# Kernel optimization log

Hardware: AMD Instinct MI355X
Metric: run time of the kernel (lower is better)

## Reference

```python
import jax, jax.numpy as jnp
from jax import lax
import numpy as np

B, T, H, L = 4096, 7, 512, 256
D = 2 * H  # bidirectional LSTM feature dim


def _lstm(x, wih, whh, bih, bhh, reverse):
    # x: [B, T, L]; torch gate order i, f, g, o
    b, hdim = x.shape[0], whh.shape[0]
    xs = jnp.swapaxes(x, 0, 1)  # [T, B, L]
    bias = bih + bhh

    def step(carry, xt):
        h, c = carry
        gates = xt @ wih + h @ whh + bias
        i, f, g, o = jnp.split(gates, 4, axis=-1)
        c = jax.nn.sigmoid(f) * c + jax.nn.sigmoid(i) * jnp.tanh(g)
        h = jax.nn.sigmoid(o) * jnp.tanh(c)
        return (h, c), h

    h0 = jnp.zeros((b, hdim), x.dtype)
    _, hs = lax.scan(step, (h0, h0), xs, reverse=reverse)
    return jnp.swapaxes(hs, 0, 1)  # [B, T, H]


def _att(enc, dec):
    # Sequential attention: keys/values start as enc and grow with each decoder output.
    keys = enc  # [B, T, D]
    outs = []
    for i in range(dec.shape[1]):  # fixed small T=7, Python loop is static
        q = dec[:, i, :]                                  # [B, D]
        scores = jnp.einsum('bd,btd->bt', q, keys)        # dot over features
        a = jax.nn.softmax(scores, axis=1)
        ctx = jnp.einsum('bt,btd->bd', a, keys)
        out = ctx + q
        outs.append(out)
        keys = jnp.concatenate([keys, out[:, None, :]], axis=1)
    return jnp.stack(outs, axis=1)  # [B, T, D]


def _deconv(x, w, b):
    # torch ConvTranspose2d (stride 1, pad 0) == full conv with flipped, in/out-swapped kernel
    kh, kw = w.shape[2], w.shape[3]
    w2 = jnp.transpose(w[:, :, ::-1, ::-1], (1, 0, 2, 3))  # [out, in, kh, kw]
    y = lax.conv_general_dilated(x, w2, (1, 1), ((kh - 1, kh - 1), (kw - 1, kw - 1)),
                                 dimension_numbers=('NCHW', 'OIHW', 'NCHW'))
    return y + b[None, :, None, None]


def setup_inputs() -> dict:
    key = jax.random.key(0)
    ks = jax.random.split(key, 12)
    p = lambda k, shape: jax.random.normal(k, shape, jnp.float32) * 0.02
    return {
        'lstm_enc': jax.random.normal(ks[0], (B, T, D), jnp.float32),
        'gaussian_noise': jax.random.normal(ks[1], (B, L), jnp.float32),
        'embedrep_w': p(ks[2], (L, L * T)), 'embedrep_b': jnp.zeros((L * T,), jnp.float32),
        'wih_f': p(ks[3], (L, 4 * H)), 'whh_f': p(ks[4], (H, 4 * H)),
        'bih_f': jnp.zeros((4 * H,), jnp.float32), 'bhh_f': jnp.zeros((4 * H,), jnp.float32),
        'wih_b': p(ks[5], (L, 4 * H)), 'whh_b': p(ks[6], (H, 4 * H)),
        'bih_b': jnp.zeros((4 * H,), jnp.float32), 'bhh_b': jnp.zeros((4 * H,), jnp.float32),
        'emb_w': p(ks[7], (D, 1024)), 'emb_b': jnp.zeros((1024,), jnp.float32),
        'dc3_w': p(ks[8], (64, 32, 1, 3)), 'dc3_b': jnp.zeros((32,), jnp.float32),
        'dc1_w': p(ks[9], (32, 16, 1, 5)), 'dc1_b': jnp.zeros((16,), jnp.float32),
        'dc2_w': p(ks[10], (16, 1, 3, 3)), 'dc2_b': jnp.zeros((1,), jnp.float32),
        'infer': 0,
    }


def reference(lstm_enc, gaussian_noise, embedrep_w, embedrep_b,
              wih_f, whh_f, bih_f, bhh_f, wih_b, whh_b, bih_b, bhh_b,
              emb_w, emb_b, dc3_w, dc3_b, dc1_w, dc1_b, dc2_w, dc2_b, infer):
    b = lstm_enc.shape[0]
    g1 = jax.nn.soft_sign(gaussian_noise @ embedrep_w + embedrep_b)   # [B, L*T]
    rep = g1.reshape(b, T, L)                                          # [B, 7, L]
    hf = _lstm(rep, wih_f, whh_f, bih_f, bhh_f, False)
    hb = _lstm(rep, wih_b, whh_b, bih_b, bhh_b, True)
    lstm1 = jnp.concatenate([hf, hb], axis=-1)                         # [B, 7, 2H]
    att_out = _att(lstm_enc, lstm1)                                    # [B, 7, 2H]
    emb = att_out @ emb_w + emb_b                                      # [B, 7, 1024]
    up = jax.nn.soft_sign(emb).reshape(b * T, 64, 1, 16)
    x = jax.nn.leaky_relu(_deconv(up, dc3_w, dc3_b))                   # [B*7, 32, 1, 18]
    x = jax.nn.leaky_relu(_deconv(x, dc1_w, dc1_b))                    # [B*7, 16, 1, 22]
    x = jax.nn.leaky_relu(_deconv(x, dc2_w, dc2_b))                    # [B*7, 1, 3, 24]
    x = jax.nn.softmax(x, axis=2)                                      # softmax over H dim (=3)
    out = x.reshape(b, T, 1, 3, 24)[:, :, -1, :, :]                    # [B, 7, 3, 24]
    return out
```

## Files before the change

kernel.cpp:

```cpp
#include <hip/hip_runtime.h>
#include <stdint.h>


typedef __attribute__((ext_vector_type(4))) float f32x4;
typedef __attribute__((ext_vector_type(8))) short bf16x8;
typedef __attribute__((ext_vector_type(4))) unsigned short us4;

__device__ __forceinline__ unsigned short f2b(float f) {
  union { float f; unsigned u; } x; x.f = f;
  unsigned r = x.u + 0x7FFFu + ((x.u >> 16) & 1u);
  return (unsigned short)(r >> 16);
}
__device__ __forceinline__ float b2f(unsigned short s) {
  union { unsigned u; float f; } x; x.u = ((unsigned)s) << 16; return x.f;
}
__device__ __forceinline__ float sigmoidf(float x) {
  return 1.f / (1.f + __expf(-x));
}
__device__ __forceinline__ float fast_tanh(float x) {
  x = fminf(15.f, fmaxf(-15.f, x));
  float e = __expf(2.f * x);
  return (e - 1.f) / (e + 1.f);
}

__device__ __forceinline__ void gl_lds16(const void* g, void* l) {
  auto gp = reinterpret_cast<const __attribute__((address_space(1))) unsigned int*>(
      reinterpret_cast<uintptr_t>(g));
  auto lp = reinterpret_cast<__attribute__((address_space(3))) unsigned int*>(
      reinterpret_cast<uintptr_t>(l));
  __builtin_amdgcn_global_load_lds(gp, lp, 16, 0, 0);
}


__device__ __forceinline__ void stage_half(const unsigned short* src, int ld,
                                           unsigned short* hbase, int tid) {
  const int row_in = tid >> 2;
  const int gidx = tid & 3;
#pragma unroll
  for (int r = 0; r < 2; ++r) {
    int row = r * 128 + row_in;
    int gsrc = gidx ^ ((row >> 1) & 3);
    gl_lds16(src + (size_t)row * ld + gsrc * 8, hbase + r * 4096 + (tid >> 6) * 512);
  }
}

__device__ __forceinline__ bf16x8 lds_fragH(const unsigned short* hbase, int row, int lq) {
  return *(const bf16x8*)(hbase + row * 32 + (lq ^ (((row >> 1) & 3) << 3)));
}

__device__ __forceinline__ void tile_reads(const unsigned short* Ab, const unsigned short* Bb,
                                           int wm, int wn, int lane,
                                           bf16x8 (&a)[8], bf16x8 (&b)[4]) {
  const int lr = lane & 15, lq = (lane >> 4) * 8;
#pragma unroll
  for (int i = 0; i < 8; ++i) a[i] = lds_fragH(Ab, wm * 128 + i * 16 + lr, lq);
#pragma unroll
  for (int n = 0; n < 4; ++n) b[n] = lds_fragH(Bb, wn * 64 + n * 16 + lr, lq);
}

__device__ __forceinline__ void tile_mfma(bf16x8 (&a)[8], bf16x8 (&b)[4], f32x4 (&acc)[8][4]) {
  __builtin_amdgcn_s_setprio(1);
#pragma unroll
  for (int i = 0; i < 8; ++i)
#pragma unroll
    for (int n = 0; n < 4; ++n)
      acc[i][n] = __builtin_amdgcn_mfma_f32_16x16x32_bf16(a[i], b[n], acc[i][n], 0, 0, 0);
  __builtin_amdgcn_s_setprio(0);
}

#define RING_TOP(t, NT)                                                   \
  if ((t) < (NT)-2) asm volatile("s_waitcnt vmcnt(4)" ::: "memory");      \
  else              asm volatile("s_waitcnt vmcnt(0)" ::: "memory");      \
  __builtin_amdgcn_s_barrier();                                           \
  __builtin_amdgcn_sched_barrier(0);                                      \
  asm volatile("s_waitcnt lgkmcnt(0)" ::: "memory");                      \
  __builtin_amdgcn_sched_barrier(0);

__device__ __forceinline__ void stage128x64(const unsigned short* src, int ld,
                                            unsigned short* lds, int wv, int lane) {
#pragma unroll
  for (int r = 0; r < 4; ++r) {
    int row = r * 32 + wv * 8 + (lane >> 3);
    gl_lds16(src + (size_t)row * ld + (lane & 7) * 8, lds + (r * 32 + wv * 8) * 64);
  }
}
__device__ __forceinline__ void mfma_tile(const unsigned short* As, const unsigned short* Bs,
                                          int wm, int wn, int lane, f32x4 acc[4][4]) {
#pragma unroll
  for (int kk = 0; kk < 2; ++kk) {
    int ko = kk * 32 + (lane >> 4) * 8;
    bf16x8 a[4], b[4];
#pragma unroll
    for (int i = 0; i < 4; ++i)
      a[i] = *(const bf16x8*)(As + (size_t)(wm * 64 + i * 16 + (lane & 15)) * 64 + ko);
#pragma unroll
    for (int i = 0; i < 4; ++i)
      b[i] = *(const bf16x8*)(Bs + (size_t)(wn * 64 + i * 16 + (lane & 15)) * 64 + ko);
#pragma unroll
    for (int mi = 0; mi < 4; ++mi)
#pragma unroll
      for (int ni = 0; ni < 4; ++ni)
        acc[mi][ni] = __builtin_amdgcn_mfma_f32_16x16x32_bf16(a[mi], b[ni], acc[mi][ni], 0, 0, 0);
  }
}

__global__ __launch_bounds__(256) void pack_kernel(
    const float* __restrict__ noise, const float* __restrict__ erep_w,
    const float* __restrict__ emb_w,
    const float* __restrict__ wih_f, const float* __restrict__ whh_f,
    const float* __restrict__ bih_f, const float* __restrict__ bhh_f,
    const float* __restrict__ wih_b, const float* __restrict__ whh_b,
    const float* __restrict__ bih_b, const float* __restrict__ bhh_b,
    unsigned short* __restrict__ noiseb, unsigned short* __restrict__ erepT,
    unsigned short* __restrict__ embT, unsigned short* __restrict__ lstmW,
    float* __restrict__ lstmB) {
  const int N0 = 4096 * 256;
  const int N1 = 1792 * 256;
  const int N2 = 1024 * 1024;
  const int N3 = 2 * 2048 * 768;
  const int N4 = 2 * 2048;
  const int total = N0 + N1 + N2 + N3 + N4;
  for (int i = blockIdx.x * 256 + threadIdx.x; i < total; i += gridDim.x * 256) {
    int x = i;
    if (x < N0) { noiseb[x] = f2b(noise[x]); continue; }
    x -= N0;
    if (x < N1) { int n = x >> 8, k = x & 255; erepT[x] = f2b(erep_w[k * 1792 + n]); continue; }
    x -= N1;
    if (x < N2) {
      int n = x >> 10, k = x & 1023;
      int o = (n & 63) * 16 + (n >> 6);
      embT[x] = f2b(emb_w[k * 1024 + o]);
      continue;
    }
    x -= N2;
    if (x < N3) {
      int dir = x / (2048 * 768);
      int r = x - dir * (2048 * 768);
      int npk = r / 768, k = r - (r / 768) * 768;
      int blk = npk >> 6, g = (npk >> 4) & 3, u = npk & 15;
      int o = g * 512 + blk * 16 + u;
      const float* wih = dir ? wih_b : wih_f;
      const float* whh = dir ? whh_b : whh_f;
      float v = (k < 256) ? wih[k * 2048 + o] : whh[(k - 256) * 2048 + o];
      lstmW[x] = f2b(v);
      continue;
    }
    x -= N3;
    {
      int dir = x >> 11, npk = x & 2047;
      int blk = npk >> 6, g = (npk >> 4) & 3, u = npk & 15;
      int o = g * 512 + blk * 16 + u;
      lstmB[x] = dir ? (bih_b[o] + bhh_b[o]) : (bih_f[o] + bhh_f[o]);
    }
  }
}

__global__ __launch_bounds__(256) void gemm_rep_kernel(
    const unsigned short* __restrict__ A, const unsigned short* __restrict__ Bt,
    const float* __restrict__ bias, unsigned short* __restrict__ rep_t) {
  __shared__ unsigned short As[128 * 64];
  __shared__ unsigned short Bs[128 * 64];
  const int lane = threadIdx.x & 63, wv = threadIdx.x >> 6;
  const int wm = wv >> 1, wn = wv & 1;
  const int m0 = blockIdx.y * 128, n0 = blockIdx.x * 128;
  f32x4 acc[4][4];
#pragma unroll
  for (int i = 0; i < 4; ++i)
#pragma unroll
    for (int j = 0; j < 4; ++j) acc[i][j] = (f32x4){0.f, 0.f, 0.f, 0.f};
  for (int k0 = 0; k0 < 256; k0 += 64) {
    stage128x64(A + (size_t)m0 * 256 + k0, 256, As, wv, lane);
    stage128x64(Bt + (size_t)n0 * 256 + k0, 256, Bs, wv, lane);
    __syncthreads();
    mfma_tile(As, Bs, wm, wn, lane, acc);
    __syncthreads();
  }
#pragma unroll
  for (int ni = 0; ni < 4; ++ni) {
    int n = n0 + wn * 64 + ni * 16 + (lane & 15);
    float bv = bias[n];
    int t = n >> 8, l = n & 255;
#pragma unroll
    for (int mi = 0; mi < 4; ++mi)
#pragma unroll
      for (int r = 0; r < 4; ++r) {
        int m = m0 + wm * 64 + mi * 16 + (lane >> 4) * 4 + r;
        float v = acc[mi][ni][r] + bv;
        v = v / (1.f + fabsf(v));
        rep_t[((size_t)t * 4096 + m) * 256 + l] = f2b(v);
      }
  }
}

__global__ __launch_bounds__(512, 2) void lstm_step256_kernel(
    const unsigned short* __restrict__ rep_t, const unsigned short* __restrict__ Wp,
    const float* __restrict__ biasP, unsigned short* __restrict__ hbuf,
    unsigned short* __restrict__ cbuf, unsigned short* __restrict__ lstm1, int step) {
  __shared__ unsigned short Ar[4][8192];
  __shared__ unsigned short Br[4][8192];
  const int tid = threadIdx.x, lane = tid & 63, wv = tid >> 6;
  const int wm = wv >> 2, wn = wv & 3;
  const int swz = (blockIdx.x & 7) * 32 + (blockIdx.x >> 3);
  const int dir = swz >> 7;
  const int by = (swz & 127) >> 3, bx = swz & 7;
  const int m0 = by * 256, n0 = bx * 256;
  const int t_proc = dir ? (6 - step) : step;
  const unsigned short* W = Wp + (size_t)dir * 2048 * 768;
  const unsigned short* hin = hbuf + ((size_t)(step & 1) * 2 + dir) * (4096 * 512);
  unsigned short* hout = hbuf + ((size_t)((step + 1) & 1) * 2 + dir) * (4096 * 512);
  unsigned short* cp = cbuf + (size_t)dir * (4096 * 512);
  const unsigned short* xsrc = rep_t + (size_t)t_proc * 4096 * 256;

  f32x4 acc[8][4];
#pragma unroll
  for (int i = 0; i < 8; ++i)
#pragma unroll
    for (int j = 0; j < 4; ++j) acc[i][j] = (f32x4){0.f, 0.f, 0.f, 0.f};

  auto asrc = [&](int tt) {
    return tt < 8 ? xsrc + (size_t)m0 * 256 + tt * 32
                  : hin + (size_t)m0 * 512 + (tt - 8) * 32;
  };
  auto ald = [&](int tt) { return tt < 8 ? 256 : 512; };

  stage_half(asrc(0), ald(0), Ar[0], tid);
  stage_half(W + (size_t)n0 * 768 + 0 * 32, 768, Br[0], tid);
  stage_half(asrc(1), ald(1), Ar[1], tid);
  stage_half(W + (size_t)n0 * 768 + 1 * 32, 768, Br[1], tid);
  stage_half(asrc(2), ald(2), Ar[2], tid);
  stage_half(W + (size_t)n0 * 768 + 2 * 32, 768, Br[2], tid);
  asm volatile("s_waitcnt vmcnt(8)" ::: "memory");
  __builtin_amdgcn_s_barrier();
  __builtin_amdgcn_sched_barrier(0);
  bf16x8 a[8], b[4];
  tile_reads(Ar[0], Br[0], wm, wn, lane, a, b);

  for (int t = 0; t < 24; ++t) {
    RING_TOP(t, 24)
    tile_mfma(a, b, acc);
    if (t + 3 < 24) {
      stage_half(asrc(t + 3), ald(t + 3), Ar[(t + 3) & 3], tid);
      stage_half(W + (size_t)n0 * 768 + (t + 3) * 32, 768, Br[(t + 3) & 3], tid);
    }
    if (t + 1 < 24) tile_reads(Ar[(t + 1) & 3], Br[(t + 1) & 3], wm, wn, lane, a, b);
  }

  const int u = lane & 15;
  const int blk = (n0 + wn * 64) >> 6;
  const int j = blk * 16 + u;
  const float bz0 = biasP[dir * 2048 + blk * 64 + 0 * 16 + u];
  const float bz1 = biasP[dir * 2048 + blk * 64 + 1 * 16 + u];
  const float bz2 = biasP[dir * 2048 + blk * 64 + 2 * 16 + u];
  const float bz3 = biasP[dir * 2048 + blk * 64 + 3 * 16 + u];
#pragma unroll
  for (int mi = 0; mi < 8; ++mi)
#pragma unroll
    for (int r = 0; r < 4; ++r) {
      int row = m0 + wm * 128 + mi * 16 + (lane >> 4) * 4 + r;
      float gi = acc[mi][0][r] + bz0;
      float gf = acc[mi][1][r] + bz1;
      float gg = acc[mi][2][r] + bz2;
      float go = acc[mi][3][r] + bz3;
      size_t ci = (size_t)row * 512 + j;
      float c = sigmoidf(gf) * b2f(cp[ci]) + sigmoidf(gi) * fast_tanh(gg);
      cp[ci] = f2b(c);
      float h = sigmoidf(go) * fast_tanh(c);
      unsigned short hb = f2b(h);
      hout[ci] = hb;
      lstm1[((size_t)row * 7 + t_proc) * 1024 + dir * 512 + j] = hb;
    }
}

__global__ __launch_bounds__(256) void att_fused3_kernel(
    const float* __restrict__ enc, const unsigned short* __restrict__ lstm1,
    unsigned short* __restrict__ att) {
  __shared__ unsigned short Qs[7 * 1032];
  __shared__ unsigned short Es[7 * 1032];
  __shared__ float P[8 * 256];
  __shared__ float sG[98];
  __shared__ float sC[7][14];
  __shared__ float sA[16];
  const int tid = threadIdx.x, lane = tid & 63, wv = tid >> 6;
  const int b = blockIdx.x;
  const float* Eb = enc + (size_t)b * 7168;
  const unsigned short* Qb = lstm1 + (size_t)b * 7168;

  if (tid < 98) ((float*)sC)[tid] = 0.f;

  const f32x4* Eb4 = (const f32x4*)Eb;
  const int d0 = tid * 4;
#pragma unroll
  for (int r = 0; r < 7; ++r) {
    f32x4 v = Eb4[r * 256 + tid];
    us4 hi;
#pragma unroll
    for (int e = 0; e < 4; ++e) hi[e] = f2b(v[e]);
    *(us4*)&Es[r * 1032 + d0] = hi;
    *(us4*)&Qs[r * 1032 + d0] = *(const us4*)(Qb + r * 1024 + d0);
  }
  asm volatile("s_waitcnt lgkmcnt(0)" ::: "memory");
  __builtin_amdgcn_sched_barrier(0);

  {
    const int rr = lane & 15;
    const int rowc = rr % 7;
    const int kbase = wv * 256 + (lane >> 4) * 8;
    f32x4 g1 = {0.f, 0.f, 0.f, 0.f}, g2 = {0.f, 0.f, 0.f, 0.f};
#pragma unroll
    for (int s = 0; s < 8; ++s) {
      const int k0 = kbase + s * 32;
      bf16x8 aq = *(const bf16x8*)&Qs[rowc * 1032 + k0];
      bf16x8 be = *(const bf16x8*)&Es[rowc * 1032 + k0];
      g1 = __builtin_amdgcn_mfma_f32_16x16x32_bf16(aq, be, g1, 0, 0, 0);
      g2 = __builtin_amdgcn_mfma_f32_16x16x32_bf16(aq, aq, g2, 0, 0, 0);
    }
    *(f32x4*)&P[((wv * 2 + 0) * 64 + lane) * 4] = g1;
    *(f32x4*)&P[((wv * 2 + 1) * 64 + lane) * 4] = g2;
  }
  __syncthreads();

  if (tid < 98) {
    int i = tid / 14, v = tid - i * 14;
    int col = v < 7 ? v : v - 7;
    int tile = v < 7 ? 0 : 1;
    int ln = ((i >> 2) << 4) | col;
    int rg = i & 3;
    float s = 0.f;
#pragma unroll
    for (int w = 0; w < 4; ++w) s += P[((w * 2 + tile) * 64 + ln) * 4 + rg];
    sG[i * 14 + v] = s;
  }
  __syncthreads();
  if (wv == 0) {
    for (int i = 0; i < 7; ++i) {
      const int nt = 7 + i;
      float s = -1e30f;
      if (lane < 7) {
        s = sG[i * 14 + lane];
      } else if (lane < nt) {
        int jj = lane - 7;
        float a2 = 0.f;
#pragma unroll
        for (int v = 0; v < 14; ++v) a2 += sC[jj][v] * sG[i * 14 + v];
        s = a2;
      }
      float mx = s;
#pragma unroll
      for (int off = 8; off >= 1; off >>= 1) mx = fmaxf(mx, __shfl_xor(mx, off, 16));
      float e = (lane < nt) ? __expf(s - mx) : 0.f;
      float sum = e;
#pragma unroll
      for (int off = 8; off >= 1; off >>= 1) sum += __shfl_xor(sum, off, 16);
      float aw = e / sum;
      if (lane < 16) sA[lane] = aw;
      if (lane < 14) {
        float c = (lane < 7) ? sA[lane] : 0.f;
        for (int jj = 0; jj < i; ++jj) c += sA[7 + jj] * sC[jj][lane];
        if (lane == 7 + i) c += 1.f;
        sC[i][lane] = c;
      }
    }
  }
  __syncthreads();

  {
    float acc[7][4];
#pragma unroll
    for (int i = 0; i < 7; ++i)
#pragma unroll
      for (int e = 0; e < 4; ++e) acc[i][e] = 0.f;
#pragma unroll
    for (int t = 0; t < 7; ++t) {
      us4 ev = *(const us4*)&Es[t * 1032 + d0];
      float evf[4];
#pragma unroll
      for (int e = 0; e < 4; ++e) evf[e] = b2f(ev[e]);
#pragma unroll
      for (int i = 0; i < 7; ++i) {
        float c = sC[i][t];
#pragma unroll
        for (int e = 0; e < 4; ++e) acc[i][e] += c * evf[e];
      }
    }
#pragma unroll
    for (int m = 0; m < 7; ++m) {
      us4 qv = *(const us4*)&Qs[m * 1032 + d0];
      float qf[4];
#pragma unroll
      for (int e = 0; e < 4; ++e) qf[e] = b2f(qv[e]);
#pragma unroll
      for (int i = m; i < 7; ++i) {
        float c = sC[i][7 + m];
#pragma unroll
        for (int e = 0; e < 4; ++e) acc[i][e] += c * qf[e];
      }
    }
    unsigned short* Ab = att + (size_t)b * 7168;
#pragma unroll
    for (int i = 0; i < 7; ++i) {
      us4 r;
#pragma unroll
      for (int e = 0; e < 4; ++e) r[e] = f2b(acc[i][e]);
      *(us4*)(Ab + i * 1024 + d0) = r;
    }
  }
}

__global__ __launch_bounds__(512, 2) void gemm_emb256_kernel(
    const unsigned short* __restrict__ A, const unsigned short* __restrict__ Bt,
    const float* __restrict__ bias, unsigned short* __restrict__ up_t) {
  __shared__ unsigned short Ar[4][8192];
  __shared__ unsigned short Br[4][8192];
  const int tid = threadIdx.x, lane = tid & 63, wv = tid >> 6;
  const int wm = wv >> 2, wn = wv & 3;
  const int swz = (blockIdx.x & 7) * 56 + (blockIdx.x >> 3);
  const int by = swz >> 2, bx = swz & 3;
  const int m0 = by * 256, n0 = bx * 256;

  f32x4 acc[8][4];
#pragma unroll
  for (int i = 0; i < 8; ++i)
#pragma unroll
    for (int j = 0; j < 4; ++j) acc[i][j] = (f32x4){0.f, 0.f, 0.f, 0.f};

  const unsigned short* Abase = A + (size_t)m0 * 1024;
  const unsigned short* Bbase = Bt + (size_t)n0 * 1024;

  stage_half(Abase + 0 * 32, 1024, Ar[0], tid);
  stage_half(Bbase + 0 * 32, 1024, Br[0], tid);
  stage_half(Abase + 1 * 32, 1024, Ar[1], tid);
  stage_half(Bbase + 1 * 32, 1024, Br[1], tid);
  stage_half(Abase + 2 * 32, 1024, Ar[2], tid);
  stage_half(Bbase + 2 * 32, 1024, Br[2], tid);
  asm volatile("s_waitcnt vmcnt(8)" ::: "memory");
  __builtin_amdgcn_s_barrier();
  __builtin_amdgcn_sched_barrier(0);
  bf16x8 a[8], b[4];
  tile_reads(Ar[0], Br[0], wm, wn, lane, a, b);

  for (int t = 0; t < 32; ++t) {
    RING_TOP(t, 32)
    tile_mfma(a, b, acc);
    if (t + 3 < 32) {
      stage_half(Abase + (t + 3) * 32, 1024, Ar[(t + 3) & 3], tid);
      stage_half(Bbase + (t + 3) * 32, 1024, Br[(t + 3) & 3], tid);
    }
    if (t + 1 < 32) tile_reads(Ar[(t + 1) & 3], Br[(t + 1) & 3], wm, wn, lane, a, b);
  }

#pragma unroll
  for (int ni = 0; ni < 4; ++ni) {
    int np = n0 + wn * 64 + ni * 16 + (lane & 15);
    int o = (np & 63) * 16 + (np >> 6);
    float bv = bias[o];
#pragma unroll
    for (int mi = 0; mi < 8; ++mi)
#pragma unroll
      for (int r = 0; r < 4; ++r) {
        int m = m0 + wm * 128 + mi * 16 + (lane >> 4) * 4 + r;
        float v = acc[mi][ni][r] + bv;
        v = v / (1.f + fabsf(v));
        up_t[(size_t)m * 1024 + np] = f2b(v);
      }
  }
}

__global__ __launch_bounds__(256) void dc3_kernel(const unsigned short* __restrict__ up_t,
                                                  const float* __restrict__ w3,
                                                  const float* __restrict__ b3,
                                                  unsigned short* __restrict__ y1_t) {
  const int lane = threadIdx.x & 63, wv = threadIdx.x >> 6;
  const int kq = (lane >> 4) * 8;
  const int oc = lane & 15;
  bf16x8 bf[2][6];
#pragma unroll
  for (int nt = 0; nt < 2; ++nt)
#pragma unroll
    for (int kk = 0; kk < 6; ++kk) {
      bf16x8 v;
#pragma unroll
      for (int t = 0; t < 8; ++t) {
        int k = kk * 32 + kq + t;
        int jj = k >> 6, ic = k & 63;
        v[t] = (short)f2b(w3[((size_t)ic * 32 + nt * 16 + oc) * 3 + jj]);
      }
      bf[nt][kk] = v;
    }
  const float bia0 = b3[oc], bia1 = b3[16 + oc];
  const int base_chunk = blockIdx.x * 32 + wv * 8;
  for (int cc = 0; cc < 8; ++cc) {
    const int chunk = base_chunk + cc;
    int m = chunk * 16 + (lane & 15);
    int img = m / 18, ow = m - img * 18;
    const unsigned short* arow = up_t + (size_t)img * 1024;
    f32x4 acc0 = {0.f, 0.f, 0.f, 0.f}, acc1 = {0.f, 0.f, 0.f, 0.f};
#pragma unroll
    for (int kk = 0; kk < 6; ++kk) {
      int jj = kk >> 1;
      int ic0 = (kk & 1) * 32 + kq;
      int iw = ow - jj;
      bf16x8 a = {0, 0, 0, 0, 0, 0, 0, 0};
      if ((unsigned)iw < 16u) a = *(const bf16x8*)(arow + iw * 64 + ic0);
      acc0 = __builtin_amdgcn_mfma_f32_16x16x32_bf16(a, bf[0][kk], acc0, 0, 0, 0);
      acc1 = __builtin_amdgcn_mfma_f32_16x16x32_bf16(a, bf[1][kk], acc1, 0, 0, 0);
    }
#pragma unroll
    for (int r = 0; r < 4; ++r) {
      int mm = chunk * 16 + (lane >> 4) * 4 + r;
      float v0 = acc0[r] + bia0; v0 = v0 > 0.f ? v0 : 0.01f * v0;
      float v1 = acc1[r] + bia1; v1 = v1 > 0.f ? v1 : 0.01f * v1;
      y1_t[(size_t)mm * 32 + oc] = f2b(v0);
      y1_t[(size_t)mm * 32 + 16 + oc] = f2b(v1);
    }
  }
}

__global__ __launch_bounds__(256) void dc1_kernel(const unsigned short* __restrict__ y1_t,
                                                  const float* __restrict__ w1,
                                                  const float* __restrict__ b1,
                                                  unsigned short* __restrict__ y2_t) {
  const int lane = threadIdx.x & 63, wv = threadIdx.x >> 6;
  const int kq = (lane >> 4) * 8;
  const int oc = lane & 15;
  bf16x8 bf[5];
#pragma unroll
  for (int kk = 0; kk < 5; ++kk) {
    bf16x8 v;
#pragma unroll
    for (int t = 0; t < 8; ++t) {
      int ic = kq + t;
      v[t] = (short)f2b(w1[((size_t)ic * 16 + oc) * 5 + kk]);
    }
    bf[kk] = v;
  }
  const float bia = b1[oc];
  const int base_chunk = blockIdx.x * 32 + wv * 8;
  for (int cc = 0; cc < 8; ++cc) {
    const int chunk = base_chunk + cc;
    int m = chunk * 16 + (lane & 15);
    int img = m / 22, ow = m - img * 22;
    const unsigned short* abase = y1_t + (size_t)img * 18 * 32;
    f32x4 acc = {0.f, 0.f, 0.f, 0.f};
#pragma unroll
    for (int kk = 0; kk < 5; ++kk) {
      int iw = ow - kk;
      bf16x8 a = {0, 0, 0, 0, 0, 0, 0, 0};
      if ((unsigned)iw < 18u) a = *(const bf16x8*)(abase + iw * 32 + kq);
      acc = __builtin_amdgcn_mfma_f32_16x16x32_bf16(a, bf[kk], acc, 0, 0, 0);
    }
#pragma unroll
    for (int r = 0; r < 4; ++r) {
      int mm = chunk * 16 + (lane >> 4) * 4 + r;
      float v = acc[r] + bia;
      v = v > 0.f ? v : 0.01f * v;
      y2_t[(size_t)mm * 16 + oc] = f2b(v);
    }
  }
}

__global__ __launch_bounds__(256) void dc2_kernel(const unsigned short* __restrict__ y2_t,
                                                  const float* __restrict__ w2,
                                                  const float* __restrict__ b2,
                                                  float* __restrict__ out) {
  int idx = blockIdx.x * 256 + threadIdx.x;
  int img = idx / 24, ow = idx - img * 24;
  float lg0 = b2[0], lg1 = b2[0], lg2 = b2[0];
#pragma unroll
  for (int jj = 0; jj < 3; ++jj) {
    int iw = ow - jj;
    if ((unsigned)iw >= 22u) continue;
    const unsigned short* row = y2_t + ((size_t)img * 22 + iw) * 16;
    bf16x8 v0 = *(const bf16x8*)(row);
    bf16x8 v1 = *(const bf16x8*)(row + 8);
    float x[16];
#pragma unroll
    for (int ic = 0; ic < 8; ++ic) {
      x[ic] = b2f((unsigned short)v0[ic]);
      x[8 + ic] = b2f((unsigned short)v1[ic]);
    }
#pragma unroll
    for (int ic = 0; ic < 16; ++ic) {
      lg0 += x[ic] * w2[ic * 9 + 0 * 3 + jj];
      lg1 += x[ic] * w2[ic * 9 + 1 * 3 + jj];
      lg2 += x[ic] * w2[ic * 9 + 2 * 3 + jj];
    }
  }
  lg0 = lg0 > 0.f ? lg0 : 0.01f * lg0;
  lg1 = lg1 > 0.f ? lg1 : 0.01f * lg1;
  lg2 = lg2 > 0.f ? lg2 : 0.01f * lg2;
  float mx = fmaxf(lg0, fmaxf(lg1, lg2));
  float e0 = __expf(lg0 - mx), e1 = __expf(lg1 - mx), e2 = __expf(lg2 - mx);
  float inv = 1.f / (e0 + e1 + e2);
  size_t ob = (size_t)img * 72 + ow;
  out[ob] = e0 * inv;
  out[ob + 24] = e1 * inv;
  out[ob + 48] = e2 * inv;
}

extern "C" void kernel_launch(void* const* d_in, const int* in_sizes, int n_in,
                              void* d_out, int out_size, void* d_ws, size_t ws_size,
                              hipStream_t stream) {
  (void)in_sizes; (void)n_in; (void)out_size; (void)ws_size;
  const float* enc    = (const float*)d_in[0];
  const float* noise  = (const float*)d_in[1];
  const float* erep_w = (const float*)d_in[2];
  const float* erep_b = (const float*)d_in[3];
  const float* wih_f  = (const float*)d_in[4];
  const float* whh_f  = (const float*)d_in[5];
  const float* bih_f  = (const float*)d_in[6];
  const float* bhh_f  = (const float*)d_in[7];
  const float* wih_b  = (const float*)d_in[8];
  const float* whh_b  = (const float*)d_in[9];
  const float* bih_b  = (const float*)d_in[10];
  const float* bhh_b  = (const float*)d_in[11];
  const float* emb_w  = (const float*)d_in[12];
  const float* emb_b  = (const float*)d_in[13];
  const float* dc3w   = (const float*)d_in[14];
  const float* dc3b   = (const float*)d_in[15];
  const float* dc1w   = (const float*)d_in[16];
  const float* dc1b   = (const float*)d_in[17];
  const float* dc2w   = (const float*)d_in[18];
  const float* dc2b   = (const float*)d_in[19];
  float* out = (float*)d_out;

  char* p = (char*)d_ws;
  auto carve = [&p](size_t bytes) {
    char* r = p;
    p += (bytes + 255) & ~(size_t)255;
    return r;
  };
  unsigned short* rep_t  = (unsigned short*)carve(7ull * 4096 * 256 * 2);
  unsigned short* lstmW  = (unsigned short*)carve(2ull * 2048 * 768 * 2);
  float*          lstmB  = (float*)carve(2ull * 2048 * 4);
  unsigned short* noiseb = (unsigned short*)carve(4096ull * 256 * 2);
  unsigned short* erepT  = (unsigned short*)carve(1792ull * 256 * 2);
  unsigned short* embT   = (unsigned short*)carve(1024ull * 1024 * 2);
  unsigned short* hbuf   = (unsigned short*)carve(4ull * 4096 * 512 * 2);
  unsigned short* cbuf   = (unsigned short*)carve(2ull * 4096 * 512 * 2);
  unsigned short* lstm1  = (unsigned short*)carve(4096ull * 7 * 1024 * 2);
  unsigned short* att    = (unsigned short*)carve(28672ull * 1024 * 2);
  unsigned short* up_t   = (unsigned short*)carve(28672ull * 1024 * 2);
  unsigned short* y1_t   = (unsigned short*)carve(28672ull * 18 * 32 * 2);
  unsigned short* y2_t   = (unsigned short*)carve(28672ull * 22 * 16 * 2);

  hipMemsetAsync(hbuf, 0, 2ull * 4096 * 512 * 2, stream);
  hipMemsetAsync(cbuf, 0, 2ull * 4096 * 512 * 2, stream);

  pack_kernel<<<2048, 256, 0, stream>>>(noise, erep_w, emb_w, wih_f, whh_f, bih_f, bhh_f,
                                        wih_b, whh_b, bih_b, bhh_b,
                                        noiseb, erepT, embT, lstmW, lstmB);
  gemm_rep_kernel<<<dim3(14, 32), 256, 0, stream>>>(noiseb, erepT, erep_b, rep_t);
  for (int s = 0; s < 7; ++s)
    lstm_step256_kernel<<<256, 512, 0, stream>>>(rep_t, lstmW, lstmB, hbuf, cbuf, lstm1, s);
  att_fused3_kernel<<<4096, 256, 0, stream>>>(enc, lstm1, att);
  gemm_emb256_kernel<<<448, 512, 0, stream>>>(att, embT, emb_b, up_t);
  dc3_kernel<<<1008, 256, 0, stream>>>(up_t, dc3w, dc3b, y1_t);
  dc1_kernel<<<1232, 256, 0, stream>>>(y1_t, dc1w, dc1b, y2_t);
  dc2_kernel<<<2688, 256, 0, stream>>>(y2_t, dc2w, dc2b, out);
}
```

Before: 495.0 us.

## Shrink LSTM and embedding GEMM tiles to 128x128 with triple-buffered ring

Replaces the 256x256-tile, 512-thread, 4-deep LDS ring GEMMs for the LSTM step and embedding projection with 128x128 tiles, 256 threads, and a 3-stage ring that loads fragments and runs MFMAs in the same step. This gives 4x more blocks (1024 and 1792) so the wave is better balanced across CUs, and lower LDS use allows 3 blocks per CU. In exchange each block reuses less data, which raises global/L2 traffic, and the software prefetch of register fragments one stage ahead is dropped.

```diff
diff --git a/kernel.cpp b/kernel.cpp
--- a/kernel.cpp
+++ b/kernel.cpp
@@ -32,15 +32,15 @@
 }
 
 
-__device__ __forceinline__ void stage_half(const unsigned short* src, int ld,
-                                           unsigned short* hbase, int tid) {
+__device__ __forceinline__ void stage128x32(const unsigned short* src, int ld,
+                                            unsigned short* hbase, int tid) {
   const int row_in = tid >> 2;
   const int gidx = tid & 3;
 #pragma unroll
   for (int r = 0; r < 2; ++r) {
-    int row = r * 128 + row_in;
+    int row = r * 64 + row_in;
     int gsrc = gidx ^ ((row >> 1) & 3);
-    gl_lds16(src + (size_t)row * ld + gsrc * 8, hbase + r * 4096 + (tid >> 6) * 512);
+    gl_lds16(src + (size_t)row * ld + gsrc * 8, hbase + r * 2048 + (tid >> 6) * 512);
   }
 }
 
@@ -48,32 +48,27 @@
   return *(const bf16x8*)(hbase + row * 32 + (lq ^ (((row >> 1) & 3) << 3)));
 }
 
-__device__ __forceinline__ void tile_reads(const unsigned short* Ab, const unsigned short* Bb,
-                                           int wm, int wn, int lane,
-                                           bf16x8 (&a)[8], bf16x8 (&b)[4]) {
+__device__ __forceinline__ void tile16(const unsigned short* Ab, const unsigned short* Bb,
+                                       int wm, int wn, int lane, f32x4 (&acc)[4][4]) {
   const int lr = lane & 15, lq = (lane >> 4) * 8;
-#pragma unroll
-  for (int i = 0; i < 8; ++i) a[i] = lds_fragH(Ab, wm * 128 + i * 16 + lr, lq);
+  bf16x8 a[4], b[4];
+#pragma unroll
+  for (int i = 0; i < 4; ++i) a[i] = lds_fragH(Ab, wm * 64 + i * 16 + lr, lq);
 #pragma unroll
   for (int n = 0; n < 4; ++n) b[n] = lds_fragH(Bb, wn * 64 + n * 16 + lr, lq);
-}
-
-__device__ __forceinline__ void tile_mfma(bf16x8 (&a)[8], bf16x8 (&b)[4], f32x4 (&acc)[8][4]) {
   __builtin_amdgcn_s_setprio(1);
 #pragma unroll
-  for (int i = 0; i < 8; ++i)
+  for (int i = 0; i < 4; ++i)
 #pragma unroll
     for (int n = 0; n < 4; ++n)
       acc[i][n] = __builtin_amdgcn_mfma_f32_16x16x32_bf16(a[i], b[n], acc[i][n], 0, 0, 0);
   __builtin_amdgcn_s_setprio(0);
 }
 
-#define RING_TOP(t, NT)                                                   \
-  if ((t) < (NT)-2) asm volatile("s_waitcnt vmcnt(4)" ::: "memory");      \
-  else              asm volatile("s_waitcnt vmcnt(0)" ::: "memory");      \
+#define R3TOP(t, NT)                                                      \
+  if ((t) + 1 < (NT)) asm volatile("s_waitcnt vmcnt(4)" ::: "memory");    \
+  else                asm volatile("s_waitcnt vmcnt(0)" ::: "memory");    \
   __builtin_amdgcn_s_barrier();                                           \
-  __builtin_amdgcn_sched_barrier(0);                                      \
-  asm volatile("s_waitcnt lgkmcnt(0)" ::: "memory");                      \
   __builtin_amdgcn_sched_barrier(0);
 
 __device__ __forceinline__ void stage128x64(const unsigned short* src, int ld,
@@ -192,18 +187,19 @@
   }
 }
 
-__global__ __launch_bounds__(512, 2) void lstm_step256_kernel(
+__global__ __launch_bounds__(256, 3) void lstm_step128_kernel(
     const unsigned short* __restrict__ rep_t, const unsigned short* __restrict__ Wp,
     const float* __restrict__ biasP, unsigned short* __restrict__ hbuf,
     unsigned short* __restrict__ cbuf, unsigned short* __restrict__ lstm1, int step) {
-  __shared__ unsigned short Ar[4][8192];
-  __shared__ unsigned short Br[4][8192];
+  __shared__ unsigned short Ar[3][4096];
+  __shared__ unsigned short Br[3][4096];
   const int tid = threadIdx.x, lane = tid & 63, wv = tid >> 6;
-  const int wm = wv >> 2, wn = wv & 3;
-  const int swz = (blockIdx.x & 7) * 32 + (blockIdx.x >> 3);
-  const int dir = swz >> 7;
-  const int by = (swz & 127) >> 3, bx = swz & 7;
-  const int m0 = by * 256, n0 = bx * 256;
+  const int wm = wv >> 1, wn = wv & 1;
+  const int swz = (blockIdx.x & 7) * 128 + (blockIdx.x >> 3);
+  const int dir = swz >> 9;
+  const int rem = swz & 511;
+  const int by = rem >> 4, bx = rem & 15;
+  const int m0 = by * 128, n0 = bx * 128;
   const int t_proc = dir ? (6 - step) : step;
   const unsigned short* W = Wp + (size_t)dir * 2048 * 768;
   const unsigned short* hin = hbuf + ((size_t)(step & 1) * 2 + dir) * (4096 * 512);
@@ -211,9 +207,9 @@
   unsigned short* cp = cbuf + (size_t)dir * (4096 * 512);
   const unsigned short* xsrc = rep_t + (size_t)t_proc * 4096 * 256;
 
-  f32x4 acc[8][4];
-#pragma unroll
-  for (int i = 0; i < 8; ++i)
+  f32x4 acc[4][4];
+#pragma unroll
+  for (int i = 0; i < 4; ++i)
 #pragma unroll
     for (int j = 0; j < 4; ++j) acc[i][j] = (f32x4){0.f, 0.f, 0.f, 0.f};
 
@@ -223,26 +219,19 @@
   };
   auto ald = [&](int tt) { return tt < 8 ? 256 : 512; };
 
-  stage_half(asrc(0), ald(0), Ar[0], tid);
-  stage_half(W + (size_t)n0 * 768 + 0 * 32, 768, Br[0], tid);
-  stage_half(asrc(1), ald(1), Ar[1], tid);
-  stage_half(W + (size_t)n0 * 768 + 1 * 32, 768, Br[1], tid);
-  stage_half(asrc(2), ald(2), Ar[2], tid);
-  stage_half(W + (size_t)n0 * 768 + 2 * 32, 768, Br[2], tid);
-  asm volatile("s_waitcnt vmcnt(8)" ::: "memory");
-  __builtin_amdgcn_s_barrier();
-  __builtin_amdgcn_sched_barrier(0);
-  bf16x8 a[8], b[4];
-  tile_reads(Ar[0], Br[0], wm, wn, lane, a, b);
-
+  stage128x32(asrc(0), ald(0), Ar[0], tid);
+  stage128x32(W + (size_t)n0 * 768 + 0 * 32, 768, Br[0], tid);
+  stage128x32(asrc(1), ald(1), Ar[1], tid);
+  stage128x32(W + (size_t)n0 * 768 + 1 * 32, 768, Br[1], tid);
+
+#pragma unroll
   for (int t = 0; t < 24; ++t) {
-    RING_TOP(t, 24)
-    tile_mfma(a, b, acc);
-    if (t + 3 < 24) {
-      stage_half(asrc(t + 3), ald(t + 3), Ar[(t + 3) & 3], tid);
-      stage_half(W + (size_t)n0 * 768 + (t + 3) * 32, 768, Br[(t + 3) & 3], tid);
-    }
-    if (t + 1 < 24) tile_reads(Ar[(t + 1) & 3], Br[(t + 1) & 3], wm, wn, lane, a, b);
+    R3TOP(t, 24)
+    if (t + 2 < 24) {
+      stage128x32(asrc(t + 2), ald(t + 2), Ar[(t + 2) % 3], tid);
+      stage128x32(W + (size_t)n0 * 768 + (t + 2) * 32, 768, Br[(t + 2) % 3], tid);
+    }
+    tile16(Ar[t % 3], Br[t % 3], wm, wn, lane, acc);
   }
 
   const int u = lane & 15;
@@ -253,10 +242,10 @@
   const float bz2 = biasP[dir * 2048 + blk * 64 + 2 * 16 + u];
   const float bz3 = biasP[dir * 2048 + blk * 64 + 3 * 16 + u];
 #pragma unroll
-  for (int mi = 0; mi < 8; ++mi)
+  for (int mi = 0; mi < 4; ++mi)
 #pragma unroll
     for (int r = 0; r < 4; ++r) {
-      int row = m0 + wm * 128 + mi * 16 + (lane >> 4) * 4 + r;
+      int row = m0 + wm * 64 + mi * 16 + (lane >> 4) * 4 + r;
       float gi = acc[mi][0][r] + bz0;
       float gf = acc[mi][1][r] + bz1;
       float gg = acc[mi][2][r] + bz2;
@@ -406,46 +395,39 @@
   }
 }
 
-__global__ __launch_bounds__(512, 2) void gemm_emb256_kernel(
+__global__ __launch_bounds__(256, 3) void gemm_emb128_kernel(
     const unsigned short* __restrict__ A, const unsigned short* __restrict__ Bt,
     const float* __restrict__ bias, unsigned short* __restrict__ up_t) {
-  __shared__ unsigned short Ar[4][8192];
-  __shared__ unsigned short Br[4][8192];
+  __shared__ unsigned short Ar[3][4096];
+  __shared__ unsigned short Br[3][4096];
   const int tid = threadIdx.x, lane = tid & 63, wv = tid >> 6;
-  const int wm = wv >> 2, wn = wv & 3;
-  const int swz = (blockIdx.x & 7) * 56 + (blockIdx.x >> 3);
-  const int by = swz >> 2, bx = swz & 3;
-  const int m0 = by * 256, n0 = bx * 256;
-
-  f32x4 acc[8][4];
-#pragma unroll
-  for (int i = 0; i < 8; ++i)
+  const int wm = wv >> 1, wn = wv & 1;
+  const int swz = (blockIdx.x & 7) * 224 + (blockIdx.x >> 3);
+  const int by = swz >> 3, bx = swz & 7;
+  const int m0 = by * 128, n0 = bx * 128;
+
+  f32x4 acc[4][4];
+#pragma unroll
+  for (int i = 0; i < 4; ++i)
 #pragma unroll
     for (int j = 0; j < 4; ++j) acc[i][j] = (f32x4){0.f, 0.f, 0.f, 0.f};
 
   const unsigned short* Abase = A + (size_t)m0 * 1024;
   const unsigned short* Bbase = Bt + (size_t)n0 * 1024;
 
-  stage_half(Abase + 0 * 32, 1024, Ar[0], tid);
-  stage_half(Bbase + 0 * 32, 1024, Br[0], tid);
-  stage_half(Abase + 1 * 32, 1024, Ar[1], tid);
-  stage_half(Bbase + 1 * 32, 1024, Br[1], tid);
-  stage_half(Abase + 2 * 32, 1024, Ar[2], tid);
-  stage_half(Bbase + 2 * 32, 1024, Br[2], tid);
-  asm volatile("s_waitcnt vmcnt(8)" ::: "memory");
-  __builtin_amdgcn_s_barrier();
-  __builtin_amdgcn_sched_barrier(0);
-  bf16x8 a[8], b[4];
-  tile_reads(Ar[0], Br[0], wm, wn, lane, a, b);
-
+  stage128x32(Abase + 0 * 32, 1024, Ar[0], tid);
+  stage128x32(Bbase + 0 * 32, 1024, Br[0], tid);
+  stage128x32(Abase + 1 * 32, 1024, Ar[1], tid);
+  stage128x32(Bbase + 1 * 32, 1024, Br[1], tid);
+
+#pragma unroll
   for (int t = 0; t < 32; ++t) {
-    RING_TOP(t, 32)
-    tile_mfma(a, b, acc);
-    if (t + 3 < 32) {
-      stage_half(Abase + (t + 3) * 32, 1024, Ar[(t + 3) & 3], tid);
-      stage_half(Bbase + (t + 3) * 32, 1024, Br[(t + 3) & 3], tid);
-    }
-    if (t + 1 < 32) tile_reads(Ar[(t + 1) & 3], Br[(t + 1) & 3], wm, wn, lane, a, b);
+    R3TOP(t, 32)
+    if (t + 2 < 32) {
+      stage128x32(Abase + (t + 2) * 32, 1024, Ar[(t + 2) % 3], tid);
+      stage128x32(Bbase + (t + 2) * 32, 1024, Br[(t + 2) % 3], tid);
+    }
+    tile16(Ar[t % 3], Br[t % 3], wm, wn, lane, acc);
   }
 
 #pragma unroll
@@ -454,10 +436,10 @@
     int o = (np & 63) * 16 + (np >> 6);
     float bv = bias[o];
 #pragma unroll
-    for (int mi = 0; mi < 8; ++mi)
+    for (int mi = 0; mi < 4; ++mi)
 #pragma unroll
       for (int r = 0; r < 4; ++r) {
-        int m = m0 + wm * 128 + mi * 16 + (lane >> 4) * 4 + r;
+        int m = m0 + wm * 64 + mi * 16 + (lane >> 4) * 4 + r;
         float v = acc[mi][ni][r] + bv;
         v = v / (1.f + fabsf(v));
         up_t[(size_t)m * 1024 + np] = f2b(v);
@@ -651,9 +633,9 @@
                                         noiseb, erepT, embT, lstmW, lstmB);
   gemm_rep_kernel<<<dim3(14, 32), 256, 0, stream>>>(noiseb, erepT, erep_b, rep_t);
   for (int s = 0; s < 7; ++s)
-    lstm_step256_kernel<<<256, 512, 0, stream>>>(rep_t, lstmW, lstmB, hbuf, cbuf, lstm1, s);
+    lstm_step128_kernel<<<1024, 256, 0, stream>>>(rep_t, lstmW, lstmB, hbuf, cbuf, lstm1, s);
   att_fused3_kernel<<<4096, 256, 0, stream>>>(enc, lstm1, att);
-  gemm_emb256_kernel<<<448, 512, 0, stream>>>(att, embT, emb_b, up_t);
+  gemm_emb128_kernel<<<1792, 256, 0, stream>>>(att, embT, emb_b, up_t);
   dc3_kernel<<<1008, 256, 0, stream>>>(up_t, dc3w, dc3b, y1_t);
   dc1_kernel<<<1232, 256, 0, stream>>>(y1_t, dc1w, dc1b, y2_t);
   dc2_kernel<<<2688, 256, 0, stream>>>(y2_t, dc2w, dc2b, out);
```

Result: no change. 502.2 us (+1.5%).
